# Kernel optimization log

Measured on AMD Instinct MI355X. Metric: run time of the kernel, lower is better.

## Reference

```python
import jax, jax.numpy as jnp
import numpy as np


def setup_inputs() -> dict:
    key = jax.random.key(0)
    k1, k2, k3, k4 = jax.random.split(key, 4)
    N, F_in, F_out = 8192, 512, 256
    inp = jax.random.normal(k1, (N, F_in), dtype=jnp.float32)
    adj = jax.random.uniform(k2, (N, N), dtype=jnp.float32)
    stdv = 1.0 / np.sqrt(F_out)
    weight = jax.random.uniform(k3, (F_in, F_out), minval=-stdv, maxval=stdv, dtype=jnp.float32)
    b = jax.random.uniform(k4, (F_out,), minval=-stdv, maxval=stdv, dtype=jnp.float32)
    return {"input": inp, "adj": adj, "weight": weight, "b": b}


def reference(input, adj, weight, b):
    N = adj.shape[0]
    degree = jnp.sum(adj, axis=1)                      # [N]
    # A_tilde = 2*I - adj
    A_tilde = 2.0 * jnp.eye(N, dtype=adj.dtype) - adj
    d_inv_sqrt = 1.0 / jnp.sqrt(2.0 + degree)          # [N]
    # D^-1/2 @ A_tilde @ D^-1/2 as broadcasted row/col scaling (same math, O(N^2))
    L_sharpen = d_inv_sqrt[:, None] * A_tilde * d_inv_sqrt[None, :]
    support = input @ weight                           # [N, F_out]
    out = L_sharpen @ support + b                      # [N, F_out]
    return jax.nn.relu(out)
```

## Files before the change

kernel.cpp:

```cpp
#include <hip/hip_runtime.h>


typedef _Float16 h4 __attribute__((ext_vector_type(4)));
typedef _Float16 h8 __attribute__((ext_vector_type(8)));
typedef float f4 __attribute__((ext_vector_type(4)));

__device__ __forceinline__ void gload_lds16(const void* g, void* l) {
    __builtin_amdgcn_global_load_lds(
        (const __attribute__((address_space(1))) void*)g,
        (__attribute__((address_space(3))) void*)l, 16, 0, 0);
}
__device__ __forceinline__ void gload2(const float* p, f4& x, f4& y) {
    asm volatile("global_load_dwordx4 %0, %2, off\n\t"
                 "global_load_dwordx4 %1, %2, off offset:16"
                 : "=&v"(x), "=&v"(y) : "v"(p) : "memory");
}
__device__ __forceinline__ void gloadBfrag(const char* p, h8& x, h8& y) {
    asm volatile("global_load_dwordx4 %0, %2, off\n\t"
                 "global_load_dwordx4 %1, %2, off offset:1024"
                 : "=&v"(x), "=&v"(y) : "v"(p) : "memory");
}

__global__ __launch_bounds__(256) void k0_wt(const float* __restrict__ weight,
                                             char* __restrict__ wt) {
    const int idx = blockIdx.x * 256 + threadIdx.x;
    const int k = idx >> 8, j = idx & 255;
    const _Float16 h = (_Float16)weight[idx];
    const int off = j * 1024 + ((k >> 6) << 7) + (((k & 63) << 1) ^ ((j & 7) << 4));
    *(_Float16*)(wt + off) = h;
}

__global__ __launch_bounds__(256) void k1_deg(const float* __restrict__ adj,
                                              float* __restrict__ dinv) {
    const int r = blockIdx.x;
    const float4* rp = (const float4*)(adj + (size_t)r * 8192);
    const int t = threadIdx.x;
    float s = 0.f;
#pragma unroll
    for (int i = 0; i < 8; ++i) {
        float4 v = rp[t + i * 256];
        s += (v.x + v.y) + (v.z + v.w);
    }
#pragma unroll
    for (int off = 32; off > 0; off >>= 1) s += __shfl_down(s, off, 64);
    __shared__ float part[4];
    if ((t & 63) == 0) part[t >> 6] = s;
    __syncthreads();
    if (t == 0) {
        float deg = (part[0] + part[1]) + (part[2] + part[3]);
        dinv[r] = 1.0f / sqrtf(2.0f + deg);
    }
}

__global__ __launch_bounds__(512) void k2_support(const float* __restrict__ input,
                                                  const char* __restrict__ wt,
                                                  const float* __restrict__ dinv,
                                                  char* __restrict__ sT) {
    __shared__ char smem[4096 + 32768];
    const int t = threadIdx.x, w = t >> 6, l = t & 63;
    const int r0 = (int)blockIdx.x * 32;
    const int arow = t >> 4, ak4 = t & 15;
    const int bj = l >> 3, bb = (l & 7) * 16;

    f4 acc[2][2] = {};

    for (int kt = 0; kt < 8; ++kt) {
        const int k0 = kt * 64;
        __syncthreads();
        {
            float4 v = *(const float4*)(input + (size_t)(r0 + arow) * 512 + k0 + ak4 * 4);
            h4 h;
            h[0] = (_Float16)v.x; h[1] = (_Float16)v.y;
            h[2] = (_Float16)v.z; h[3] = (_Float16)v.w;
            *(h4*)(smem + arow * 128 + ((ak4 * 8) ^ ((arow & 7) << 4))) = h;
        }
#pragma unroll
        for (int q = 0; q < 4; ++q) {
            const int c = q * 8 + w;
            gload_lds16(wt + (size_t)(c * 8 + bj) * 1024 + kt * 128 + bb,
                        smem + 4096 + c * 1024);
        }
        __syncthreads();
#pragma unroll
        for (int kk = 0; kk < 2; ++kk) {
            const int ko = kk * 64 + ((l >> 4) << 4);
            h8 a[2], b[2];
#pragma unroll
            for (int m = 0; m < 2; ++m) {
                const int r = m * 16 + (l & 15);
                a[m] = *(const h8*)(smem + r * 128 + (ko ^ ((r & 7) << 4)));
            }
#pragma unroll
            for (int n = 0; n < 2; ++n) {
                const int j = w * 32 + n * 16 + (l & 15);
                b[n] = *(const h8*)(smem + 4096 + j * 128 + (ko ^ ((j & 7) << 4)));
            }
#pragma unroll
            for (int m = 0; m < 2; ++m)
#pragma unroll
                for (int n = 0; n < 2; ++n)
                    acc[m][n] = __builtin_amdgcn_mfma_f32_16x16x32_f16(a[m], b[n], acc[m][n], 0, 0, 0);
        }
    }
#pragma unroll
    for (int m = 0; m < 2; ++m)
#pragma unroll
        for (int n = 0; n < 2; ++n) {
            const int j = w * 32 + n * 16 + (l & 15);
            const int k0r = r0 + m * 16 + ((l >> 4) << 2);
            h4 h;
#pragma unroll
            for (int r = 0; r < 4; ++r)
                h[r] = (_Float16)(dinv[k0r + r] * acc[m][n][r]);
            const int off = (((j >> 4) * 128 + (k0r >> 6)) << 11) +
                            (((k0r >> 5) & 1) << 10) +
                            ((((k0r >> 3) & 3) << 4) + (j & 15)) * 16 +
                            ((k0r & 7) << 1);
            *(h4*)(sT + off) = h;
        }
}

__global__ __launch_bounds__(512, 4) void k3_spmm(const float* __restrict__ adj,
                                                  const char* __restrict__ sT,
                                                  _Float16* __restrict__ parth,
                                                  float* __restrict__ out,
                                                  int steps) {
    __shared__ __align__(16) char smem[2][8192];
    const int t = threadIdx.x;
    const int w = t >> 6, l = t & 63;
    const int i0 = (int)blockIdx.x * 64;
    const int ks0 = (int)blockIdx.y * steps * 64;
    const int dkt = (i0 - ks0) >> 6;

    const int arow = t >> 3;
    const int ak8 = (t & 7) * 8;
    const int arow_g = i0 + arow;
    const float* aptr = adj + (size_t)arow_g * 8192 + ks0 + ak8;
    const int a_off = arow * 128 + (((t & 7) << 4) ^ ((arow & 7) << 4));

    const char* bpn0 = sT + ((size_t)(w * 2) * 128 + (ks0 >> 6)) * 2048 + l * 16;
    const char* bpn1 = bpn0 + 262144;

    f4 acc[4][2] = {};
    h8 bvA[2][2], bvB[2][2];
    f4 ax0, ay0, ax1, ay1;

    auto loadB = [&](int kt, h8 (&bv)[2][2]) {
        gloadBfrag(bpn0 + (size_t)kt * 2048, bv[0][0], bv[1][0]);
        gloadBfrag(bpn1 + (size_t)kt * 2048, bv[0][1], bv[1][1]);
    };
    auto writeA = [&](char* buf, int kt, const f4 x, const f4 y) {
        const int kg = ks0 + kt * 64 + ak8;
        h8 h;
        if (kt == dkt) {
#pragma unroll
            for (int e = 0; e < 4; ++e)
                h[e] = (_Float16)((arow_g == kg + e) ? 2.0f - x[e] : -x[e]);
#pragma unroll
            for (int e = 0; e < 4; ++e)
                h[4 + e] = (_Float16)((arow_g == kg + 4 + e) ? 2.0f - y[e] : -y[e]);
        } else {
#pragma unroll
            for (int e = 0; e < 4; ++e) h[e] = (_Float16)(-x[e]);
#pragma unroll
            for (int e = 0; e < 4; ++e) h[4 + e] = (_Float16)(-y[e]);
        }
        *(h8*)(buf + a_off) = h;
    };
    auto compute = [&](const char* A, const h8 (&bv)[2][2]) {
        __builtin_amdgcn_s_setprio(1);
#pragma unroll
        for (int kk = 0; kk < 2; ++kk) {
            const int ko = kk * 64 + ((l >> 4) << 4);
            h8 a[4];
#pragma unroll
            for (int m = 0; m < 4; ++m) {
                const int r = m * 16 + (l & 15);
                a[m] = *(const h8*)(A + r * 128 + (ko ^ ((r & 7) << 4)));
            }
#pragma unroll
            for (int m = 0; m < 4; ++m)
#pragma unroll
                for (int n = 0; n < 2; ++n)
                    acc[m][n] = __builtin_amdgcn_mfma_f32_16x16x32_f16(a[m], bv[kk][n], acc[m][n], 0, 0, 0);
        }
        __builtin_amdgcn_s_setprio(0);
    };

#define SBAR0() __builtin_amdgcn_sched_barrier(0)
#define WAIT_ADJ(N, X, Y)                                                     \
    asm volatile("s_waitcnt vmcnt(" #N ")" : "+v"(X), "+v"(Y) :: "memory");   \
    SBAR0();
#define WAIT_STEP(N, X, Y, BV)                                                \
    asm volatile("s_waitcnt vmcnt(" #N ")"                                    \
                 : "+v"(X), "+v"(Y), "+v"(BV[0][0]), "+v"(BV[0][1]),          \
                   "+v"(BV[1][0]), "+v"(BV[1][1]) :: "memory");               \
    SBAR0();
#define WAIT_BV(N, BV)                                                        \
    asm volatile("s_waitcnt vmcnt(" #N ")"                                    \
                 : "+v"(BV[0][0]), "+v"(BV[0][1]),                            \
                   "+v"(BV[1][0]), "+v"(BV[1][1]) :: "memory");               \
    SBAR0();
#define BARRIER()                                                             \
    asm volatile("s_waitcnt lgkmcnt(0)\n\ts_barrier" ::: "memory");           \
    SBAR0();

    gload2(aptr, ax0, ay0);
    loadB(0, bvA);
    WAIT_ADJ(4, ax0, ay0)
    writeA(smem[0], 0, ax0, ay0);
    gload2(aptr + 64, ax1, ay1);
    BARRIER()

#define BODY(kt, XC, YC, XN, YN, BVC, BVN, BUFC, BUFN)                        \
    {                                                                         \
        loadB((kt) + 1, BVN);                                                 \
        gload2(aptr + (size_t)((kt) + 2) * 64, XC, YC);                       \
        WAIT_STEP(6, XN, YN, BVC)                                             \
        writeA(BUFN, (kt) + 1, XN, YN);                                       \
        compute(BUFC, BVC);                                                   \
        BARRIER()                                                             \
    }

    for (int kt2 = 0; kt2 + 2 <= steps - 2; kt2 += 2) {
        BODY(kt2,     ax0, ay0, ax1, ay1, bvA, bvB, smem[0], smem[1])
        BODY(kt2 + 1, ax1, ay1, ax0, ay0, bvB, bvA, smem[1], smem[0])
    }
    {
        loadB(steps - 1, bvB);
        WAIT_STEP(4, ax1, ay1, bvA)
        writeA(smem[1], steps - 1, ax1, ay1);
        compute(smem[0], bvA);
        BARRIER()
    }
    {
        WAIT_BV(0, bvB)
        compute(smem[1], bvB);
    }
#undef BODY
#undef WAIT_ADJ
#undef WAIT_STEP
#undef WAIT_BV
#undef BARRIER
#undef SBAR0

    if (blockIdx.y == gridDim.y - 1) {
#pragma unroll
        for (int m = 0; m < 4; ++m)
#pragma unroll
            for (int n = 0; n < 2; ++n) {
                const int j = w * 32 + n * 16 + (l & 15);
                const int ib = i0 + m * 16 + ((l >> 4) << 2);
#pragma unroll
                for (int r = 0; r < 4; ++r)
                    out[(size_t)(ib + r) * 256 + j] = acc[m][n][r];
            }
    } else {
        _Float16* pslot = parth + (size_t)blockIdx.y * (8192 * 256);
#pragma unroll
        for (int m = 0; m < 4; ++m)
#pragma unroll
            for (int n = 0; n < 2; ++n) {
                const int j = w * 32 + n * 16 + (l & 15);
                const int ib = i0 + m * 16 + ((l >> 4) << 2);
#pragma unroll
                for (int r = 0; r < 4; ++r)
                    pslot[(size_t)(ib + r) * 256 + j] = (_Float16)acc[m][n][r];
            }
    }
}

__global__ __launch_bounds__(256) void k4_fin(const _Float16* __restrict__ parth,
                                              float* __restrict__ out,
                                              const float* __restrict__ dinv,
                                              const float* __restrict__ bias,
                                              int nsplit) {
    const int idx = blockIdx.x * 256 + threadIdx.x;
    float4 s = ((const float4*)out)[idx];
    for (int sp = 0; sp < nsplit - 1; ++sp) {
        const h4 p = *(const h4*)(parth + (size_t)sp * (8192 * 256) + (size_t)idx * 4);
        s.x += (float)p[0]; s.y += (float)p[1];
        s.z += (float)p[2]; s.w += (float)p[3];
    }
    const float dv = dinv[idx >> 6];
    const float4 b = ((const float4*)bias)[idx & 63];
    float4 r;
    r.x = fmaxf(dv * s.x + b.x, 0.f);
    r.y = fmaxf(dv * s.y + b.y, 0.f);
    r.z = fmaxf(dv * s.z + b.z, 0.f);
    r.w = fmaxf(dv * s.w + b.w, 0.f);
    ((float4*)out)[idx] = r;
}

extern "C" void kernel_launch(void* const* d_in, const int* in_sizes, int n_in,
                              void* d_out, int out_size, void* d_ws, size_t ws_size,
                              hipStream_t stream) {
    const float* input  = (const float*)d_in[0];
    const float* adj    = (const float*)d_in[1];
    const float* weight = (const float*)d_in[2];
    const float* bias   = (const float*)d_in[3];
    float* out = (float*)d_out;

    char* ws = (char*)d_ws;
    float*    dinv  = (float*)ws;
    char*     wt    = ws + 32768;
    char*     sT    = ws + 294912;
    _Float16* parth = (_Float16*)(ws + 294912 + 4194304);

    const size_t base = 294912 + 4194304;
    int nsplit = 1;
    if (ws_size >= base + 3ull * 4194304) nsplit = 4;
    else if (ws_size >= base + 1ull * 4194304) nsplit = 2;
    const int steps = 128 / nsplit;

    k0_wt<<<512, 256, 0, stream>>>(weight, wt);
    k1_deg<<<8192, 256, 0, stream>>>(adj, dinv);
    k2_support<<<256, 512, 0, stream>>>(input, wt, dinv, sT);
    k3_spmm<<<dim3(128, nsplit), 512, 0, stream>>>(adj, sT, parth, out, steps);
    k4_fin<<<2048, 256, 0, stream>>>(parth, out, dinv, bias, nsplit);
}
```

Before: 127.7 us.

## Fuse degree reduction into support kernel and apply column scaling in SpMM

Moves the D^-1/2 column scaling from the support GEMM epilogue into the adjacency-to-fp16 conversion inside the SpMM. The degree kernel then no longer has to finish before the support GEMM starts. The degree-sum and support-GEMM work are merged into one launch, with extra blocks doing the row reductions, which removes a launch and lets the bandwidth-bound degree pass overlap the GEMM. In exchange, the SpMM stages a slice of dinv into LDS through a direct global-to-LDS load and does an extra multiply per converted element. The LDS dinv buffer holds only 2048 entries, so it assumes the largest split factor.

Measured after the change: 120.5 us. 5.7% less time.

```diff
diff --git a/kernel.cpp b/kernel.cpp
--- a/kernel.cpp
+++ b/kernel.cpp
@@ -30,35 +30,38 @@
     *(_Float16*)(wt + off) = h;
 }
 
-__global__ __launch_bounds__(256) void k1_deg(const float* __restrict__ adj,
-                                              float* __restrict__ dinv) {
-    const int r = blockIdx.x;
-    const float4* rp = (const float4*)(adj + (size_t)r * 8192);
-    const int t = threadIdx.x;
-    float s = 0.f;
-#pragma unroll
-    for (int i = 0; i < 8; ++i) {
-        float4 v = rp[t + i * 256];
-        s += (v.x + v.y) + (v.z + v.w);
-    }
-#pragma unroll
-    for (int off = 32; off > 0; off >>= 1) s += __shfl_down(s, off, 64);
-    __shared__ float part[4];
-    if ((t & 63) == 0) part[t >> 6] = s;
-    __syncthreads();
-    if (t == 0) {
-        float deg = (part[0] + part[1]) + (part[2] + part[3]);
-        dinv[r] = 1.0f / sqrtf(2.0f + deg);
-    }
-}
-
-__global__ __launch_bounds__(512) void k2_support(const float* __restrict__ input,
-                                                  const char* __restrict__ wt,
-                                                  const float* __restrict__ dinv,
-                                                  char* __restrict__ sT) {
+__global__ __launch_bounds__(512) void k12_fused(const float* __restrict__ input,
+                                                 const float* __restrict__ adj,
+                                                 const char* __restrict__ wt,
+                                                 float* __restrict__ dinv,
+                                                 char* __restrict__ sT) {
     __shared__ char smem[4096 + 32768];
-    const int t = threadIdx.x, w = t >> 6, l = t & 63;
-    const int r0 = (int)blockIdx.x * 32;
+    const int bid = (int)blockIdx.x, t = (int)threadIdx.x;
+
+    if (bid >= 256) {
+        const int r = bid - 256;
+        const float4* rp = (const float4*)(adj + (size_t)r * 8192);
+        float s = 0.f;
+#pragma unroll
+        for (int i = 0; i < 4; ++i) {
+            float4 v = rp[t + i * 512];
+            s += (v.x + v.y) + (v.z + v.w);
+        }
+#pragma unroll
+        for (int off = 32; off > 0; off >>= 1) s += __shfl_down(s, off, 64);
+        float* part = (float*)smem;
+        if ((t & 63) == 0) part[t >> 6] = s;
+        __syncthreads();
+        if (t == 0) {
+            float deg = ((part[0] + part[1]) + (part[2] + part[3])) +
+                        ((part[4] + part[5]) + (part[6] + part[7]));
+            dinv[r] = 1.0f / sqrtf(2.0f + deg);
+        }
+        return;
+    }
+
+    const int w = t >> 6, l = t & 63;
+    const int r0 = bid * 32;
     const int arow = t >> 4, ak4 = t & 15;
     const int bj = l >> 3, bb = (l & 7) * 16;
 
@@ -111,7 +114,7 @@
             h4 h;
 #pragma unroll
             for (int r = 0; r < 4; ++r)
-                h[r] = (_Float16)(dinv[k0r + r] * acc[m][n][r]);
+                h[r] = (_Float16)acc[m][n][r];
             const int off = (((j >> 4) * 128 + (k0r >> 6)) << 11) +
                             (((k0r >> 5) & 1) << 10) +
                             ((((k0r >> 3) & 3) << 4) + (j & 15)) * 16 +
@@ -122,10 +125,12 @@
 
 __global__ __launch_bounds__(512, 4) void k3_spmm(const float* __restrict__ adj,
                                                   const char* __restrict__ sT,
+                                                  const float* __restrict__ dinvg,
                                                   _Float16* __restrict__ parth,
                                                   float* __restrict__ out,
                                                   int steps) {
     __shared__ __align__(16) char smem[2][8192];
+    __shared__ __align__(16) float sdinv[2048];
     const int t = threadIdx.x;
     const int w = t >> 6, l = t & 63;
     const int i0 = (int)blockIdx.x * 64;
@@ -150,20 +155,29 @@
         gloadBfrag(bpn1 + (size_t)kt * 2048, bv[0][1], bv[1][1]);
     };
     auto writeA = [&](char* buf, int kt, const f4 x, const f4 y) {
-        const int kg = ks0 + kt * 64 + ak8;
+        const int kb = kt * 64 + ak8;
+        const float4 d0 = *(const float4*)&sdinv[kb];
+        const float4 d1 = *(const float4*)&sdinv[kb + 4];
+        const int kg = ks0 + kb;
         h8 h;
         if (kt == dkt) {
-#pragma unroll
-            for (int e = 0; e < 4; ++e)
-                h[e] = (_Float16)((arow_g == kg + e) ? 2.0f - x[e] : -x[e]);
-#pragma unroll
-            for (int e = 0; e < 4; ++e)
-                h[4 + e] = (_Float16)((arow_g == kg + 4 + e) ? 2.0f - y[e] : -y[e]);
+            h[0] = (_Float16)(d0.x * ((arow_g == kg    ) ? 2.0f - x[0] : -x[0]));
+            h[1] = (_Float16)(d0.y * ((arow_g == kg + 1) ? 2.0f - x[1] : -x[1]));
+            h[2] = (_Float16)(d0.z * ((arow_g == kg + 2) ? 2.0f - x[2] : -x[2]));
+            h[3] = (_Float16)(d0.w * ((arow_g == kg + 3) ? 2.0f - x[3] : -x[3]));
+            h[4] = (_Float16)(d1.x * ((arow_g == kg + 4) ? 2.0f - y[0] : -y[0]));
+            h[5] = (_Float16)(d1.y * ((arow_g == kg + 5) ? 2.0f - y[1] : -y[1]));
+            h[6] = (_Float16)(d1.z * ((arow_g == kg + 6) ? 2.0f - y[2] : -y[2]));
+            h[7] = (_Float16)(d1.w * ((arow_g == kg + 7) ? 2.0f - y[3] : -y[3]));
         } else {
-#pragma unroll
-            for (int e = 0; e < 4; ++e) h[e] = (_Float16)(-x[e]);
-#pragma unroll
-            for (int e = 0; e < 4; ++e) h[4 + e] = (_Float16)(-y[e]);
+            h[0] = (_Float16)(-d0.x * x[0]);
+            h[1] = (_Float16)(-d0.y * x[1]);
+            h[2] = (_Float16)(-d0.z * x[2]);
+            h[3] = (_Float16)(-d0.w * x[3]);
+            h[4] = (_Float16)(-d1.x * y[0]);
+            h[5] = (_Float16)(-d1.y * y[1]);
+            h[6] = (_Float16)(-d1.z * y[2]);
+            h[7] = (_Float16)(-d1.w * y[3]);
         }
         *(h8*)(buf + a_off) = h;
     };
@@ -205,9 +219,12 @@
     asm volatile("s_waitcnt lgkmcnt(0)\n\ts_barrier" ::: "memory");           \
     SBAR0();
 
+    gload_lds16(dinvg + ks0 + t * 4, (char*)sdinv + w * 1024);
     gload2(aptr, ax0, ay0);
     loadB(0, bvA);
     WAIT_ADJ(4, ax0, ay0)
+    asm volatile("s_barrier" ::: "memory");
+    SBAR0();
     writeA(smem[0], 0, ax0, ay0);
     gload2(aptr + 64, ax1, ay1);
     BARRIER()
@@ -314,8 +331,7 @@
     const int steps = 128 / nsplit;
 
     k0_wt<<<512, 256, 0, stream>>>(weight, wt);
-    k1_deg<<<8192, 256, 0, stream>>>(adj, dinv);
-    k2_support<<<256, 512, 0, stream>>>(input, wt, dinv, sT);
-    k3_spmm<<<dim3(128, nsplit), 512, 0, stream>>>(adj, sT, parth, out, steps);
+    k12_fused<<<8448, 512, 0, stream>>>(input, adj, wt, dinv, sT);
+    k3_spmm<<<dim3(128, nsplit), 512, 0, stream>>>(adj, sT, dinv, parth, out, steps);
     k4_fin<<<2048, 256, 0, stream>>>(parth, out, dinv, bias, nsplit);
 }
```
